# Kernel optimization log

Measured on AMD Instinct MI355X. Metric: run time of the kernel, lower is better.

The kernel has to match this reference:

```python
import jax, jax.numpy as jnp
import numpy as np

B, N, T, D, S = 2, 16384, 2048, 128, 384
NW, WQ, H, L, NH = 512, 32, 128, 3, 4
NTOK = 33  # len(const.tokens)


def _ln(x):
    m = x.mean(-1, keepdims=True)
    v = x.var(-1, keepdims=True)
    return (x - m) * jax.lax.rsqrt(v + 1e-5)


def setup_inputs() -> dict:
    key = jax.random.key(0)
    ks = jax.random.split(key, 24)
    sc = 0.02
    a = jax.random.normal(ks[0], (B, T, S), jnp.float32)
    q = jax.random.normal(ks[1], (B, N, D), jnp.float32)
    c = jax.random.normal(ks[2], (B, N, D), jnp.float32)
    atom_dec_bias = jax.random.normal(ks[3], (B, NW, NH, WQ, H), jnp.float32) * 0.1
    # one-hot atom->token map: ~8 atoms per token
    tok_idx = jnp.arange(N) // (N // T)
    atom_to_token = jnp.tile(jax.nn.one_hot(tok_idx, T, dtype=jnp.float32)[None], (B, 1, 1))
    atom_mask = jnp.ones((B, N), jnp.float32)
    # windowed key indices: 128-atom neighborhood centered on each 32-atom window
    starts = np.clip(np.arange(NW) * WQ + WQ // 2 - H // 2, 0, N - H)
    key_idx = jnp.asarray(starts[:, None] + np.arange(H)[None, :], jnp.int32)
    nrm = lambda k, shp: jax.random.normal(k, shp, jnp.float32) * sc
    p = {
        'a_to_q_w': nrm(ks[4], (S, D)),
        'Wq': nrm(ks[5], (L, D, D)), 'Wk': nrm(ks[6], (L, D, D)), 'Wv': nrm(ks[7], (L, D, D)),
        'Wg': nrm(ks[8], (L, D, D)), 'Wo': nrm(ks[9], (L, D, D)),
        'Wcs': nrm(ks[10], (L, D, D)), 'Wcb': nrm(ks[11], (L, D, D)), 'Wog': nrm(ks[12], (L, D, D)),
        'Wcs2': nrm(ks[13], (L, D, D)), 'Wcb2': nrm(ks[14], (L, D, D)), 'Wog2': nrm(ks[15], (L, D, D)),
        'W1': nrm(ks[16], (L, D, 2 * D)), 'W2': nrm(ks[17], (L, D, 2 * D)), 'W3': nrm(ks[18], (L, 2 * D, D)),
        'ln_g': jnp.ones((D,), jnp.float32), 'ln_b': jnp.zeros((D,), jnp.float32),
        'Wpos': nrm(ks[19], (D, 3)), 'Wres': nrm(ks[20], (D, NTOK)), 'bres': jnp.zeros((NTOK,), jnp.float32),
    }
    return dict(a=a, q=q, c=c, atom_dec_bias=atom_dec_bias, atom_to_token=atom_to_token,
                atom_mask=atom_mask, key_idx=key_idx, **p)


def reference(a, q, c, atom_dec_bias, atom_to_token, atom_mask, key_idx,
              a_to_q_w, Wq, Wk, Wv, Wg, Wo, Wcs, Wcb, Wog, Wcs2, Wcb2, Wog2,
              W1, W2, W3, ln_g, ln_b, Wpos, Wres, bres):
    Bq, Nq, Dq = q.shape
    nw, h = key_idx.shape
    wq = Nq // nw
    nh = atom_dec_bias.shape[2]
    dh = Dq // nh
    # token -> atom broadcast (dense bmm over one-hot == gather)
    q = q + jnp.einsum('bnt,btd->bnd', atom_to_token, a @ a_to_q_w)
    cn = _ln(c)
    mbias = (1.0 - atom_mask[:, key_idx])[:, :, None, None, :] * -1e9  # (B,NW,1,1,H)
    depth = Wq.shape[0]
    for l in range(depth):
        # AdaLN conditioning on c
        hcur = _ln(q) * jax.nn.sigmoid(cn @ Wcs[l]) + cn @ Wcb[l]
        qh = (hcur @ Wq[l]).reshape(Bq, nw, wq, nh, dh)
        hk = hcur[:, key_idx]  # (B,NW,H,D) gather = to_keys
        kh = (hk @ Wk[l]).reshape(Bq, nw, h, nh, dh)
        vh = (hk @ Wv[l]).reshape(Bq, nw, h, nh, dh)
        scores = jnp.einsum('bwqhd,bwkhd->bwhqk', qh, kh) / (dh ** 0.5) + atom_dec_bias + mbias
        attn = jax.nn.softmax(scores, axis=-1)
        o = jnp.einsum('bwhqk,bwkhd->bwqhd', attn, vh).reshape(Bq, Nq, Dq)
        o = jax.nn.sigmoid(hcur @ Wg[l]) * o
        q = q + jax.nn.sigmoid(cn @ Wog[l]) * (o @ Wo[l])
        # conditioned transition (SwiGLU)
        h2 = _ln(q) * jax.nn.sigmoid(cn @ Wcs2[l]) + cn @ Wcb2[l]
        ff = (jax.nn.silu(h2 @ W1[l]) * (h2 @ W2[l])) @ W3[l]
        q = q + jax.nn.sigmoid(cn @ Wog2[l]) * ff
    # atom -> residue scatter_add pooling
    tok_idx = jnp.argmax(atom_to_token, axis=-1)  # (B,N) int
    src = q * atom_mask[..., None]
    nt = atom_to_token.shape[-1]
    s_feat = jax.vmap(lambda s, i: jax.ops.segment_sum(s, i, num_segments=nt))(src, tok_idx)
    res_type = s_feat @ Wres + bres
    # LayerNorm + Linear position head
    r_update = (_ln(q) * ln_g + ln_b) @ Wpos
    return (r_update, res_type)
```

## Files before the change

kernel.cpp:

```cpp
#include <hip/hip_runtime.h>

typedef unsigned short u16;
typedef u16 u16x4 __attribute__((ext_vector_type(4)));
typedef u16 u16x8 __attribute__((ext_vector_type(8)));
typedef __bf16 bf16x8 __attribute__((ext_vector_type(8)));
typedef float f32x4 __attribute__((ext_vector_type(4)));

#define B_  2
#define N_  16384
#define T_  2048
#define D_  128
#define S_  384
#define NW_ 512
#define WQ_ 32
#define H_  128
#define L_  3
#define NH_ 4
#define NTOK_ 33
#define BN_ (B_*N_)

__device__ __forceinline__ float b2f(u16 u) {
    return __builtin_bit_cast(float, ((unsigned)u) << 16);
}
__device__ __forceinline__ u16 f2b(float f) {
    unsigned x = __builtin_bit_cast(unsigned, f);
    unsigned r = x + 0x7fffu + ((x >> 16) & 1u);
    return (u16)(r >> 16);
}
__device__ __forceinline__ float sigf(float x) { return 1.f / (1.f + __expf(-x)); }
__device__ __forceinline__ float ldin(const void* p, size_t i, int f) {
    return f ? ((const float*)p)[i] : b2f(((const u16*)p)[i]);
}

enum { M_STORE = 0, M_CBSG = 1, M_F32 = 2, M_RESID = 3, M_RESLN = 4 };

__global__ void sentinel_k(float* out, float v) { if (threadIdx.x == 0) out[0] = v; }

__global__ __launch_bounds__(64) void detect_k(const u16* __restrict__ a, int* flag)
{
    int t = threadIdx.x;
    u16 u = a[2 * t];
    int e = (u >> 7) & 0xFF;
    bool inval = (u != 0) && (e < 96 || e > 143);
    unsigned long long m = __ballot(inval);
    if (t == 0) flag[0] = (__popcll(m) >= 6) ? 1 : 0;
}

template<bool FUSE_LN>
__global__ __launch_bounds__(256) void gemm_k(
    const u16* __restrict__ A, int lda, int asrc,
    const u16* __restrict__ WT, int K,
    u16* __restrict__ C, int ldc,
    const u16* __restrict__ E1, int e1ld,
    float* __restrict__ QF,
    const u16* __restrict__ SG, const u16* __restrict__ CB, int sgcbld,
    u16* __restrict__ HC, int mode, const int* __restrict__ dtf)
{
    __shared__ __align__(16) char smem[FUSE_LN ? 65536 : 36864];
    u16 (*As)[72] = (u16(*)[72])smem;
    u16 (*Bs)[72] = (u16(*)[72])(smem + 18432);
    float (*Tf)[128] = (float(*)[128])smem;

    const int tid = threadIdx.x;
    const int m0 = blockIdx.x * 128, n0 = blockIdx.y * 128;
    const int lane = tid & 63, wid = tid >> 6;
    const int wr = (wid >> 1) * 64, wc = (wid & 1) * 64;
    const int lr = lane & 15, lq = lane >> 4;
    const int af32 = (asrc == 1 && dtf) ? dtf[0] : 0;

    f32x4 zero4 = {0.f, 0.f, 0.f, 0.f};
    f32x4 acc[4][4];
#pragma unroll
    for (int i = 0; i < 4; ++i)
#pragma unroll
        for (int j = 0; j < 4; ++j) acc[i][j] = zero4;

    for (int kt = 0; kt < K; kt += 64) {
#pragma unroll
        for (int i = 0; i < 4; ++i) {
            int id = tid + i * 256;
            int r = id >> 3, c = (id & 7) * 8;
            if (asrc == 2) {
                size_t ab = (size_t)(m0 + r) * 512 + kt + c;
                u16x8 u1 = *(const u16x8*)&A[ab];
                u16x8 u2 = *(const u16x8*)&A[ab + 256];
                u16x8 t;
#pragma unroll
                for (int j = 0; j < 8; ++j) {
                    float x = b2f(u1[j]);
                    t[j] = f2b(x * sigf(x) * b2f(u2[j]));
                }
                *(u16x8*)&As[r][c] = t;
            } else if (af32) {
                const float* Af = (const float*)A;
                size_t ai = (size_t)(m0 + r) * lda + kt + c;
                f32x4 p0 = *(const f32x4*)&Af[ai];
                f32x4 p1 = *(const f32x4*)&Af[ai + 4];
                u16x8 t;
                t[0] = f2b(p0[0]); t[1] = f2b(p0[1]); t[2] = f2b(p0[2]); t[3] = f2b(p0[3]);
                t[4] = f2b(p1[0]); t[5] = f2b(p1[1]); t[6] = f2b(p1[2]); t[7] = f2b(p1[3]);
                *(u16x8*)&As[r][c] = t;
            } else {
                *(u16x8*)&As[r][c] = *(const u16x8*)&A[(size_t)(m0 + r) * lda + kt + c];
            }
            *(u16x8*)&Bs[r][c] = *(const u16x8*)&WT[(size_t)(n0 + r) * K + kt + c];
        }
        __syncthreads();
#pragma unroll
        for (int ks = 0; ks < 2; ++ks) {
            bf16x8 af[4], bfr[4];
#pragma unroll
            for (int t = 0; t < 4; ++t) {
                af[t]  = *(const bf16x8*)&As[wr + t * 16 + lr][ks * 32 + lq * 8];
                bfr[t] = *(const bf16x8*)&Bs[wc + t * 16 + lr][ks * 32 + lq * 8];
            }
#pragma unroll
            for (int mt = 0; mt < 4; ++mt)
#pragma unroll
                for (int nt = 0; nt < 4; ++nt)
                    acc[mt][nt] = __builtin_amdgcn_mfma_f32_16x16x32_bf16(
                        bfr[nt], af[mt], acc[mt][nt], 0, 0, 0);
        }
        __syncthreads();
    }

    const bool sig_half = (n0 >= 768);
#pragma unroll
    for (int mt = 0; mt < 4; ++mt)
#pragma unroll
        for (int nt = 0; nt < 4; ++nt) {
            int lm = wr + mt * 16 + lr;
            int lnb = wc + nt * 16 + lq * 4;
            int m = m0 + lm;
            size_t o = (size_t)m * ldc + n0 + lnb;
            f32x4 v = acc[mt][nt];
            if (mode == M_STORE) {
                u16x4 t = {f2b(v[0]), f2b(v[1]), f2b(v[2]), f2b(v[3])};
                *(u16x4*)&C[o] = t;
            } else if (mode == M_CBSG) {
                u16x4 t;
#pragma unroll
                for (int r = 0; r < 4; ++r) t[r] = f2b(sig_half ? sigf(v[r]) : v[r]);
                *(u16x4*)&C[o] = t;
            } else if (mode == M_F32) {
                *(f32x4*)&QF[o] = v;
            } else {
                f32x4 q = *(const f32x4*)&QF[o];
                u16x4 e = *(const u16x4*)&E1[(size_t)m * e1ld + n0 + lnb];
#pragma unroll
                for (int r = 0; r < 4; ++r) q[r] += b2f(e[r]) * v[r];
                *(f32x4*)&QF[o] = q;
                if (FUSE_LN) *(f32x4*)&Tf[lm][lnb] = q;
            }
        }

    if (FUSE_LN && mode == M_RESLN) {
        __syncthreads();
        int g = tid >> 4, li = tid & 15;
#pragma unroll
        for (int rr = 0; rr < 8; ++rr) {
            int lm = g * 8 + rr;
            float x[8];
            float s = 0.f, sq = 0.f;
#pragma unroll
            for (int j = 0; j < 8; ++j) {
                x[j] = Tf[lm][li * 8 + j];
                s += x[j]; sq += x[j] * x[j];
            }
#pragma unroll
            for (int off = 1; off < 16; off <<= 1) {
                s  += __shfl_xor(s, off, 64);
                sq += __shfl_xor(sq, off, 64);
            }
            float mu = s * (1.f / 128.f);
            float var = sq * (1.f / 128.f) - mu * mu;
            float inv = rsqrtf(fmaxf(var, 0.f) + 1e-5f);
            int grow = m0 + lm;
            size_t sb = (size_t)grow * sgcbld;
            u16x8 hv;
#pragma unroll
            for (int j = 0; j < 8; ++j) {
                int col = li * 8 + j;
                hv[j] = f2b((x[j] - mu) * inv * b2f(SG[sb + col]) + b2f(CB[sb + col]));
            }
            *(u16x8*)&HC[(size_t)grow * 128 + li * 8] = hv;
        }
    }
}

__global__ __launch_bounds__(256) void attn_k(
    const u16* __restrict__ proj,
    const u16* __restrict__ biasbf,
    const void* __restrict__ mask,
    const int* __restrict__ key_idx,
    u16* __restrict__ o_out,
    const int* __restrict__ dtf)
{
    __shared__ __align__(16) u16 Ks[128][128];
    __shared__ __align__(16) u16 Vt[128][128];
    const int tid = threadIdx.x;
    const int b = blockIdx.x >> 9, w = blockIdx.x & 511;
    int raw = key_idx[w * 128];
    if ((unsigned)raw > (unsigned)(N_ - H_))
        raw = (int)__builtin_bit_cast(float, raw);
    const int ks0 = raw < 0 ? 0 : (raw > N_ - H_ ? N_ - H_ : raw);
    const int lane = tid & 63, h = tid >> 6;
    const int lr = lane & 15, lq = lane >> 4;
    const int hoff = h * 32;
    const int f = dtf[0];

#pragma unroll
    for (int i = 0; i < 8; ++i) {
        int id = tid + i * 256;
        int r = id >> 4, c = (id & 15) * 8;
        size_t gbase = ((size_t)(b * N_ + ks0 + r)) * 512;
        *(u16x8*)&Ks[r][c] = *(const u16x8*)&proj[gbase + 128 + c];
        u16x8 v = *(const u16x8*)&proj[gbase + 256 + c];
#pragma unroll
        for (int j = 0; j < 8; ++j) Vt[c + j][r] = v[j];
    }
    __syncthreads();

    bf16x8 aq[2];
#pragma unroll
    for (int mt = 0; mt < 2; ++mt) {
        int qa = w * 32 + mt * 16 + lr;
        aq[mt] = *(const bf16x8*)&proj[((size_t)(b * N_ + qa)) * 512 + hoff + lq * 8];
    }
    f32x4 zero4 = {0.f, 0.f, 0.f, 0.f};
    f32x4 s[2][8];
#pragma unroll
    for (int nt = 0; nt < 8; ++nt) {
        bf16x8 bk = *(const bf16x8*)&Ks[nt * 16 + lr][hoff + lq * 8];
        s[0][nt] = __builtin_amdgcn_mfma_f32_16x16x32_bf16(aq[0], bk, zero4, 0, 0, 0);
        s[1][nt] = __builtin_amdgcn_mfma_f32_16x16x32_bf16(aq[1], bk, zero4, 0, 0, 0);
    }

    const float scl = 0.17677669529663687f;
    float mb[8];
#pragma unroll
    for (int nt = 0; nt < 8; ++nt)
        mb[nt] = (1.f - ldin(mask, (size_t)b * N_ + ks0 + nt * 16 + lr, f)) * -1e9f;
    size_t bb = (((size_t)b * 512 + w) * 4 + h) * (size_t)(32 * 128);
#pragma unroll
    for (int mt = 0; mt < 2; ++mt)
#pragma unroll
        for (int nt = 0; nt < 8; ++nt)
#pragma unroll
            for (int r = 0; r < 4; ++r) {
                int qq = mt * 16 + lq * 4 + r;
                int kk = nt * 16 + lr;
                s[mt][nt][r] = s[mt][nt][r] * scl + b2f(biasbf[bb + qq * 128 + kk]) + mb[nt];
            }

#pragma unroll
    for (int mt = 0; mt < 2; ++mt)
#pragma unroll
        for (int r = 0; r < 4; ++r) {
            float mx = -3.4e38f;
#pragma unroll
            for (int nt = 0; nt < 8; ++nt) mx = fmaxf(mx, s[mt][nt][r]);
#pragma unroll
            for (int off = 1; off < 16; off <<= 1) mx = fmaxf(mx, __shfl_xor(mx, off, 64));
            float sm = 0.f;
#pragma unroll
            for (int nt = 0; nt < 8; ++nt) {
                float p = __expf(s[mt][nt][r] - mx);
                s[mt][nt][r] = p; sm += p;
            }
#pragma unroll
            for (int off = 1; off < 16; off <<= 1) sm += __shfl_xor(sm, off, 64);
            float inv = 1.f / sm;
#pragma unroll
            for (int nt = 0; nt < 8; ++nt) s[mt][nt][r] *= inv;
        }

    __syncthreads();
#pragma unroll
    for (int mt = 0; mt < 2; ++mt)
#pragma unroll
        for (int nt = 0; nt < 8; ++nt)
#pragma unroll
            for (int r = 0; r < 4; ++r)
                Ks[hoff + mt * 16 + lq * 4 + r][nt * 16 + lr] = f2b(s[mt][nt][r]);
    __syncthreads();

    f32x4 o[2][2];
    o[0][0] = zero4; o[0][1] = zero4; o[1][0] = zero4; o[1][1] = zero4;
#pragma unroll
    for (int kst = 0; kst < 4; ++kst) {
        bf16x8 ap[2], bv[2];
#pragma unroll
        for (int mt = 0; mt < 2; ++mt)
            ap[mt] = *(const bf16x8*)&Ks[hoff + mt * 16 + lr][kst * 32 + lq * 8];
#pragma unroll
        for (int nt = 0; nt < 2; ++nt)
            bv[nt] = *(const bf16x8*)&Vt[hoff + nt * 16 + lr][kst * 32 + lq * 8];
#pragma unroll
        for (int mt = 0; mt < 2; ++mt)
#pragma unroll
            for (int nt = 0; nt < 2; ++nt)
                o[mt][nt] = __builtin_amdgcn_mfma_f32_16x16x32_bf16(ap[mt], bv[nt], o[mt][nt], 0, 0, 0);
    }

#pragma unroll
    for (int mt = 0; mt < 2; ++mt)
#pragma unroll
        for (int nt = 0; nt < 2; ++nt)
#pragma unroll
            for (int r = 0; r < 4; ++r) {
                int qa = w * 32 + mt * 16 + lq * 4 + r;
                int d = hoff + nt * 16 + lr;
                size_t gi = ((size_t)(b * N_ + qa)) * 512 + 384 + d;
                float g = sigf(b2f(proj[gi]));
                o_out[((size_t)(b * N_ + qa)) * 128 + d] = f2b(g * o[mt][nt][r]);
            }
}

struct TJob { const void* base; int off; int dst; int K; int N; };
struct TJobs { TJob j[43]; };
__global__ __launch_bounds__(256) void prologue_k(
    const void* __restrict__ bias_in, u16* __restrict__ biasbf,
    const void* __restrict__ c_in, u16* __restrict__ cn,
    TJobs jobs, u16* __restrict__ wt, const int* __restrict__ dtf)
{
    __shared__ __align__(16) u16 Ls[64][72];
    int bx = blockIdx.x;
    int f = dtf[0];
    if (bx < 8192) {
        size_t i = ((size_t)bx * 256 + threadIdx.x) * 8;
        if (f) {
            const float* s = (const float*)bias_in;
            f32x4 p0 = *(const f32x4*)&s[i];
            f32x4 p1 = *(const f32x4*)&s[i + 4];
            u16x8 t;
            t[0] = f2b(p0[0]); t[1] = f2b(p0[1]); t[2] = f2b(p0[2]); t[3] = f2b(p0[3]);
            t[4] = f2b(p1[0]); t[5] = f2b(p1[1]); t[6] = f2b(p1[2]); t[7] = f2b(p1[3]);
            *(u16x8*)&biasbf[i] = t;
        } else {
            *(u16x8*)&biasbf[i] = *(const u16x8*)&((const u16*)bias_in)[i];
        }
    } else if (bx < 16384) {
        int row = (bx - 8192) * 4 + (threadIdx.x >> 6);
        int l = threadIdx.x & 63;
        size_t base = (size_t)row * 128;
        float a = ldin(c_in, base + l, f), b = ldin(c_in, base + l + 64, f);
        float s = a + b, ss = a * a + b * b;
#pragma unroll
        for (int off = 1; off < 64; off <<= 1) {
            s  += __shfl_xor(s, off, 64);
            ss += __shfl_xor(ss, off, 64);
        }
        float m = s * (1.f / 128.f);
        float v = ss * (1.f / 128.f) - m * m;
        float inv = rsqrtf(fmaxf(v, 0.f) + 1e-5f);
        cn[base + l]      = f2b((a - m) * inv);
        cn[base + l + 64] = f2b((b - m) * inv);
    } else {
        int t = bx - 16384;
        int jidx = t / 12, tidx = t - jidx * 12;
        TJob jb = jobs.j[jidx];
        int ntk = jb.K >> 6, ntn = jb.N >> 6;
        if (tidx >= ntk * ntn) return;
        int kt = (tidx % ntk) << 6;
        int nt = (tidx / ntk) << 6;
        int r = threadIdx.x >> 3, cc = (threadIdx.x & 7) * 8;
#pragma unroll
        for (int p = 0; p < 2; ++p) {
            int kl = r + p * 32;
            size_t si = (size_t)jb.off + (size_t)(kt + kl) * jb.N + nt + cc;
            u16x8 v;
            if (f) {
                const float* s = (const float*)jb.base;
                f32x4 p0 = *(const f32x4*)&s[si];
                f32x4 p1 = *(const f32x4*)&s[si + 4];
                v[0] = f2b(p0[0]); v[1] = f2b(p0[1]); v[2] = f2b(p0[2]); v[3] = f2b(p0[3]);
                v[4] = f2b(p1[0]); v[5] = f2b(p1[1]); v[6] = f2b(p1[2]); v[7] = f2b(p1[3]);
            } else {
                v = *(const u16x8*)&((const u16*)jb.base)[si];
            }
            *(u16x8*)&Ls[kl][cc] = v;
        }
        __syncthreads();
#pragma unroll
        for (int p = 0; p < 2; ++p) {
            int nl = r + p * 32;
            u16x8 w;
#pragma unroll
            for (int j = 0; j < 8; ++j) w[j] = Ls[cc + j][nl];
            *(u16x8*)&wt[(size_t)jb.dst + (size_t)(nt + nl) * jb.K + kt + cc] = w;
        }
    }
}

__global__ __launch_bounds__(256) void initq_ln_k(
    const void* __restrict__ qin, const float* __restrict__ aw,
    float* __restrict__ qf,
    const u16* __restrict__ cs0, const u16* __restrict__ cb0, int sgcbld,
    u16* __restrict__ hcur, const int* __restrict__ dtf)
{
    int an = blockIdx.x * 4 + (threadIdx.x >> 6);
    int l = threadIdx.x & 63;
    int f = dtf[0];
    int b = an >> 14, n = an & 16383, t = n >> 3;
    size_t base = (size_t)an * 128;
    size_t ab = ((size_t)b * T_ + t) * 128;
    float a0 = ldin(qin, base + l, f)      + aw[ab + l];
    float a1 = ldin(qin, base + l + 64, f) + aw[ab + l + 64];
    qf[base + l] = a0; qf[base + l + 64] = a1;
    float s = a0 + a1, ss = a0 * a0 + a1 * a1;
#pragma unroll
    for (int off = 1; off < 64; off <<= 1) {
        s  += __shfl_xor(s, off, 64);
        ss += __shfl_xor(ss, off, 64);
    }
    float m = s * (1.f / 128.f);
    float v = ss * (1.f / 128.f) - m * m;
    float inv = rsqrtf(fmaxf(v, 0.f) + 1e-5f);
    size_t sb = (size_t)an * sgcbld;
    hcur[base + l]      = f2b((a0 - m) * inv * b2f(cs0[sb + l])      + b2f(cb0[sb + l]));
    hcur[base + l + 64] = f2b((a1 - m) * inv * b2f(cs0[sb + l + 64]) + b2f(cb0[sb + l + 64]));
}

__global__ __launch_bounds__(256) void final_k(const float* __restrict__ q,
    const void* __restrict__ ln_g, const void* __restrict__ ln_b,
    const void* __restrict__ Wpos,
    const void* __restrict__ mask, const void* __restrict__ Wres,
    const void* __restrict__ bres,
    float* __restrict__ out1, float* __restrict__ out2,
    const int* __restrict__ dtf)
{
    int f = dtf[0];
    int bx = blockIdx.x;
    if (bx < 8192) {
        int row = bx * 4 + (threadIdx.x >> 6);
        int l = threadIdx.x & 63;
        size_t base = (size_t)row * 128;
        float a = q[base + l], b = q[base + l + 64];
        float s = a + b, ss = a * a + b * b;
#pragma unroll
        for (int off = 1; off < 64; off <<= 1) {
            s  += __shfl_xor(s, off, 64);
            ss += __shfl_xor(ss, off, 64);
        }
        float m = s * (1.f / 128.f);
        float v = ss * (1.f / 128.f) - m * m;
        float inv = rsqrtf(fmaxf(v, 0.f) + 1e-5f);
        float y0 = (a - m) * inv * ldin(ln_g, l, f)      + ldin(ln_b, l, f);
        float y1 = (b - m) * inv * ldin(ln_g, l + 64, f) + ldin(ln_b, l + 64, f);
        float p0 = y0 * ldin(Wpos, l * 3 + 0, f) + y1 * ldin(Wpos, (l + 64) * 3 + 0, f);
        float p1 = y0 * ldin(Wpos, l * 3 + 1, f) + y1 * ldin(Wpos, (l + 64) * 3 + 1, f);
        float p2 = y0 * ldin(Wpos, l * 3 + 2, f) + y1 * ldin(Wpos, (l + 64) * 3 + 2, f);
#pragma unroll
        for (int off = 1; off < 64; off <<= 1) {
            p0 += __shfl_xor(p0, off, 64);
            p1 += __shfl_xor(p1, off, 64);
            p2 += __shfl_xor(p2, off, 64);
        }
        if (l == 0) {
            out1[(size_t)row * 3 + 0] = p0;
            out1[(size_t)row * 3 + 1] = p1;
            out1[(size_t)row * 3 + 2] = p2;
        }
    } else {
        __shared__ float sfeat[4][128];
        int wid = threadIdx.x >> 6, l = threadIdx.x & 63;
        int tok = (bx - 8192) * 4 + wid;
        int b = tok >> 11, t = tok & 2047;
        float a0 = 0.f, a1 = 0.f;
#pragma unroll
        for (int i = 0; i < 8; ++i) {
            size_t an = (size_t)b * N_ + t * 8 + i;
            float mk = ldin(mask, an, f);
            a0 += q[an * 128 + l] * mk;
            a1 += q[an * 128 + l + 64] * mk;
        }
        sfeat[wid][l] = a0; sfeat[wid][l + 64] = a1;
        __builtin_amdgcn_s_waitcnt(0);
        if (l < NTOK_) {
            float r = ldin(bres, l, f);
            for (int d = 0; d < 128; ++d) r += sfeat[wid][d] * ldin(Wres, d * NTOK_ + l, f);
            out2[(size_t)tok * NTOK_ + l] = r;
        }
    }
}

extern "C" void kernel_launch(void* const* d_in, const int* in_sizes, int n_in,
                              void* d_out, int out_size, void* d_ws, size_t ws_size,
                              hipStream_t stream)
{
    (void)out_size;
    float* out = (float*)d_out;
    const size_t WS_NEED = 295698432;

    static const int EXP_SZ[27] = {
        1572864, 4194304, 4194304, 16777216, 67108864, 32768, 65536,
        49152, 49152, 49152, 49152, 49152, 49152,
        49152, 49152, 49152, 49152, 49152, 49152,
        98304, 98304, 98304, 128, 128, 384, 4224, 33 };
    int bad = -1;
    int ncheck = n_in < 27 ? n_in : 27;
    for (int i = 0; i < ncheck; ++i)
        if (in_sizes[i] != EXP_SZ[i]) { bad = i; break; }
    if (bad >= 0) { sentinel_k<<<1, 64, 0, stream>>>(out, 256.0f * (bad + 1)); return; }
    if (n_in < 27) { sentinel_k<<<1, 64, 0, stream>>>(out, 8192.0f); return; }
    if (ws_size < WS_NEED) { sentinel_k<<<1, 64, 0, stream>>>(out, 12288.0f); return; }

    const void* a_in    = d_in[0];
    const void* q_in    = d_in[1];
    const void* c_in    = d_in[2];
    const void* bias_in = d_in[3];
    const void* mask_in = d_in[5];
    const int*  kidx    = (const int*)d_in[6];
    const void* a2q  = d_in[7];
    const void* Wq   = d_in[8];
    const void* Wk   = d_in[9];
    const void* Wv   = d_in[10];
    const void* Wg   = d_in[11];
    const void* Wo   = d_in[12];
    const void* Wcs  = d_in[13];
    const void* Wcb  = d_in[14];
    const void* Wog  = d_in[15];
    const void* Wcs2 = d_in[16];
    const void* Wcb2 = d_in[17];
    const void* Wog2 = d_in[18];
    const void* W1   = d_in[19];
    const void* W2   = d_in[20];
    const void* W3   = d_in[21];
    const void* ln_g = d_in[22];
    const void* ln_b = d_in[23];
    const void* Wpos = d_in[24];
    const void* Wres = d_in[25];
    const void* bres = d_in[26];

    char* ws = (char*)d_ws;
    u16*   wt     = (u16*)ws;
    int*   flag   = (int*)(ws + 2088960);
    float* qf     = (float*)(ws + 2097152);
    u16*   cn     = (u16*)(ws + 18874368);
    u16*   biasbf = (u16*)(ws + 27262976);
    u16*   cnproj = (u16*)(ws + 60817408);
    u16*   hcur   = (u16*)(ws + 211812352);
    u16*   proj   = (u16*)(ws + 220200960);
    u16*   obuf   = (u16*)(ws + 253755392);
    u16*   u12    = (u16*)(ws + 262144000);
    float* aw     = (float*)(ws + 262144000);

    detect_k<<<1, 64, 0, stream>>>((const u16*)a_in, flag);

    TJobs jobs; int nj = 0;
    for (int l = 0; l < 3; ++l) {
        jobs.j[nj++] = {Wq,   l * 16384, l * 65536 + 0,     128, 128};
        jobs.j[nj++] = {Wk,   l * 16384, l * 65536 + 16384, 128, 128};
        jobs.j[nj++] = {Wv,   l * 16384, l * 65536 + 32768, 128, 128};
        jobs.j[nj++] = {Wg,   l * 16384, l * 65536 + 49152, 128, 128};
        jobs.j[nj++] = {Wcb,  l * 16384, 196608 + l * 16384,       128, 128};
        jobs.j[nj++] = {Wcb2, l * 16384, 196608 + (3 + l) * 16384, 128, 128};
        jobs.j[nj++] = {Wcs,  l * 16384, 294912 + l * 16384,       128, 128};
        jobs.j[nj++] = {Wog,  l * 16384, 294912 + (3 + l) * 16384, 128, 128};
        jobs.j[nj++] = {Wcs2, l * 16384, 294912 + (6 + l) * 16384, 128, 128};
        jobs.j[nj++] = {Wog2, l * 16384, 294912 + (9 + l) * 16384, 128, 128};
        jobs.j[nj++] = {W1,   l * 32768, 491520 + l * 65536,         128, 256};
        jobs.j[nj++] = {W2,   l * 32768, 491520 + l * 65536 + 32768, 128, 256};
        jobs.j[nj++] = {W3,   l * 32768, 688128 + l * 32768, 256, 128};
        jobs.j[nj++] = {Wo,   l * 16384, 835584 + l * 16384, 128, 128};
    }
    jobs.j[nj++] = {a2q, 0, 786432, 384, 128};

    prologue_k<<<16384 + 43 * 12, 256, 0, stream>>>(bias_in, biasbf, c_in, cn, jobs, wt, flag);
    gemm_k<false><<<dim3(32, 1), 256, 0, stream>>>(
        (const u16*)a_in, S_, 1, wt + 786432, S_, nullptr, D_,
        nullptr, 0, aw, nullptr, nullptr, 0, nullptr, M_F32, flag);
    gemm_k<false><<<dim3(256, 18), 256, 0, stream>>>(
        cn, D_, 0, wt + 196608, D_, cnproj, 2304,
        nullptr, 0, nullptr, nullptr, nullptr, 0, nullptr, M_CBSG, nullptr);
    initq_ln_k<<<8192, 256, 0, stream>>>(q_in, aw, qf,
        cnproj + 768, cnproj + 0, 2304, hcur, flag);

    for (int l = 0; l < 3; ++l) {
        const u16* wt_proj = wt + l * 65536;
        const u16* wt_w12  = wt + 491520 + l * 65536;
        const u16* wt_w3   = wt + 688128 + l * 32768;
        const u16* wt_wo   = wt + 835584 + l * 16384;
        const u16* cb2_l = cnproj + 384 + l * 128;
        const u16* og_l  = cnproj + 1152 + l * 128;
        const u16* cs2_l = cnproj + 1536 + l * 128;
        const u16* og2_l = cnproj + 1920 + l * 128;
        const u16* cs_n  = cnproj + 768 + (l + 1) * 128;
        const u16* cb_n  = cnproj + 0 + (l + 1) * 128;

        gemm_k<false><<<dim3(256, 4), 256, 0, stream>>>(
            hcur, D_, 0, wt_proj, D_, proj, 512,
            nullptr, 0, nullptr, nullptr, nullptr, 0, nullptr, M_STORE, nullptr);
        attn_k<<<1024, 256, 0, stream>>>(proj, biasbf, mask_in, kidx, obuf, flag);
        gemm_k<true><<<dim3(256, 1), 256, 0, stream>>>(
            obuf, D_, 0, wt_wo, D_, nullptr, D_,
            og_l, 2304, qf, cs2_l, cb2_l, 2304, hcur, M_RESLN, nullptr);
        gemm_k<false><<<dim3(256, 4), 256, 0, stream>>>(
            hcur, D_, 0, wt_w12, D_, u12, 512,
            nullptr, 0, nullptr, nullptr, nullptr, 0, nullptr, M_STORE, nullptr);
        if (l < 2)
            gemm_k<true><<<dim3(256, 1), 256, 0, stream>>>(
                u12, 512, 2, wt_w3, 256, nullptr, D_,
                og2_l, 2304, qf, cs_n, cb_n, 2304, hcur, M_RESLN, nullptr);
        else
            gemm_k<false><<<dim3(256, 1), 256, 0, stream>>>(
                u12, 512, 2, wt_w3, 256, nullptr, D_,
                og2_l, 2304, qf, nullptr, nullptr, 0, nullptr, M_RESID, nullptr);
    }

    final_k<<<9216, 256, 0, stream>>>(qf, ln_g, ln_b, Wpos, mask_in, Wres, bres,
                                      out, out + (size_t)BN_ * 3, flag);
}
```

Measured before the change: 981.2 us.

## Fuse follow-on projection GEMMs into residual+LayerNorm GEMM epilogue

The residual+LN GEMM epilogue now keeps the normalized 128-row tile in shared memory and immediately multiplies it by the next weight matrix (W1|W2 or the next layer's QKVG projection), writing u12/proj directly. This removes the separate projection GEMM launches and the hcur write/read round-trip. The trade-off is lower parallelism: each 128-row block now serially computes 512 output columns with only 256 blocks, instead of spreading that work over 1024 blocks.

Measured after the change: 941.4 us. 1.04x faster.

```diff
diff --git a/kernel.cpp b/kernel.cpp
--- a/kernel.cpp
+++ b/kernel.cpp
@@ -54,7 +54,8 @@
     const u16* __restrict__ E1, int e1ld,
     float* __restrict__ QF,
     const u16* __restrict__ SG, const u16* __restrict__ CB, int sgcbld,
-    u16* __restrict__ HC, int mode, const int* __restrict__ dtf)
+    u16* __restrict__ HC, int mode, const int* __restrict__ dtf,
+    const u16* __restrict__ WT2, u16* __restrict__ C2, int ldc2, int n2)
 {
     __shared__ __align__(16) char smem[FUSE_LN ? 65536 : 36864];
     u16 (*As)[72] = (u16(*)[72])smem;
@@ -157,6 +158,7 @@
     if (FUSE_LN && mode == M_RESLN) {
         __syncthreads();
         int g = tid >> 4, li = tid & 15;
+        u16x8 hvr[8];
 #pragma unroll
         for (int rr = 0; rr < 8; ++rr) {
             int lm = g * 8 + rr;
@@ -183,7 +185,62 @@
                 int col = li * 8 + j;
                 hv[j] = f2b((x[j] - mu) * inv * b2f(SG[sb + col]) + b2f(CB[sb + col]));
             }
-            *(u16x8*)&HC[(size_t)grow * 128 + li * 8] = hv;
+            hvr[rr] = hv;
+            if (HC) *(u16x8*)&HC[(size_t)grow * 128 + li * 8] = hv;
+        }
+
+        if (n2 > 0) {
+            __syncthreads();
+            u16 (*Hs)[136] = (u16(*)[136])smem;
+            u16 (*Bs2)[72] = (u16(*)[72])(smem + 36864);
+#pragma unroll
+            for (int rr = 0; rr < 8; ++rr)
+                *(u16x8*)&Hs[g * 8 + rr][li * 8] = hvr[rr];
+
+            for (int nc = 0; nc < n2; nc += 128) {
+                f32x4 acc2[4][4];
+#pragma unroll
+                for (int i = 0; i < 4; ++i)
+#pragma unroll
+                    for (int j = 0; j < 4; ++j) acc2[i][j] = zero4;
+#pragma unroll
+                for (int kt2 = 0; kt2 < 128; kt2 += 64) {
+                    __syncthreads();
+#pragma unroll
+                    for (int i = 0; i < 4; ++i) {
+                        int id = tid + i * 256;
+                        int r = id >> 3, c = (id & 7) * 8;
+                        *(u16x8*)&Bs2[r][c] =
+                            *(const u16x8*)&WT2[(size_t)(nc + r) * 128 + kt2 + c];
+                    }
+                    __syncthreads();
+#pragma unroll
+                    for (int ks = 0; ks < 2; ++ks) {
+                        bf16x8 af[4], bfr[4];
+#pragma unroll
+                        for (int t = 0; t < 4; ++t) {
+                            af[t]  = *(const bf16x8*)&Hs[wr + t * 16 + lr][kt2 + ks * 32 + lq * 8];
+                            bfr[t] = *(const bf16x8*)&Bs2[wc + t * 16 + lr][ks * 32 + lq * 8];
+                        }
+#pragma unroll
+                        for (int mt = 0; mt < 4; ++mt)
+#pragma unroll
+                            for (int nt = 0; nt < 4; ++nt)
+                                acc2[mt][nt] = __builtin_amdgcn_mfma_f32_16x16x32_bf16(
+                                    bfr[nt], af[mt], acc2[mt][nt], 0, 0, 0);
+                    }
+                }
+#pragma unroll
+                for (int mt = 0; mt < 4; ++mt)
+#pragma unroll
+                    for (int nt = 0; nt < 4; ++nt) {
+                        int m = m0 + wr + mt * 16 + lr;
+                        int n = nc + wc + nt * 16 + lq * 4;
+                        f32x4 v = acc2[mt][nt];
+                        u16x4 t = {f2b(v[0]), f2b(v[1]), f2b(v[2]), f2b(v[3])};
+                        *(u16x4*)&C2[(size_t)m * ldc2 + n] = t;
+                    }
+            }
         }
     }
 }
@@ -570,15 +627,22 @@
     prologue_k<<<16384 + 43 * 12, 256, 0, stream>>>(bias_in, biasbf, c_in, cn, jobs, wt, flag);
     gemm_k<false><<<dim3(32, 1), 256, 0, stream>>>(
         (const u16*)a_in, S_, 1, wt + 786432, S_, nullptr, D_,
-        nullptr, 0, aw, nullptr, nullptr, 0, nullptr, M_F32, flag);
+        nullptr, 0, aw, nullptr, nullptr, 0, nullptr, M_F32, flag,
+        nullptr, nullptr, 0, 0);
     gemm_k<false><<<dim3(256, 18), 256, 0, stream>>>(
         cn, D_, 0, wt + 196608, D_, cnproj, 2304,
-        nullptr, 0, nullptr, nullptr, nullptr, 0, nullptr, M_CBSG, nullptr);
+        nullptr, 0, nullptr, nullptr, nullptr, 0, nullptr, M_CBSG, nullptr,
+        nullptr, nullptr, 0, 0);
     initq_ln_k<<<8192, 256, 0, stream>>>(q_in, aw, qf,
         cnproj + 768, cnproj + 0, 2304, hcur, flag);
 
+    gemm_k<false><<<dim3(256, 4), 256, 0, stream>>>(
+        hcur, D_, 0, wt + 0 * 65536, D_, proj, 512,
+        nullptr, 0, nullptr, nullptr, nullptr, 0, nullptr, M_STORE, nullptr,
+        nullptr, nullptr, 0, 0);
+
     for (int l = 0; l < 3; ++l) {
-        const u16* wt_proj = wt + l * 65536;
+        const u16* wt_proj_n = wt + (l + 1) * 65536;
         const u16* wt_w12  = wt + 491520 + l * 65536;
         const u16* wt_w3   = wt + 688128 + l * 32768;
         const u16* wt_wo   = wt + 835584 + l * 16384;
@@ -589,24 +653,21 @@
         const u16* cs_n  = cnproj + 768 + (l + 1) * 128;
         const u16* cb_n  = cnproj + 0 + (l + 1) * 128;
 
-        gemm_k<false><<<dim3(256, 4), 256, 0, stream>>>(
-            hcur, D_, 0, wt_proj, D_, proj, 512,
-            nullptr, 0, nullptr, nullptr, nullptr, 0, nullptr, M_STORE, nullptr);
         attn_k<<<1024, 256, 0, stream>>>(proj, biasbf, mask_in, kidx, obuf, flag);
         gemm_k<true><<<dim3(256, 1), 256, 0, stream>>>(
             obuf, D_, 0, wt_wo, D_, nullptr, D_,
-            og_l, 2304, qf, cs2_l, cb2_l, 2304, hcur, M_RESLN, nullptr);
-        gemm_k<false><<<dim3(256, 4), 256, 0, stream>>>(
-            hcur, D_, 0, wt_w12, D_, u12, 512,
-            nullptr, 0, nullptr, nullptr, nullptr, 0, nullptr, M_STORE, nullptr);
+            og_l, 2304, qf, cs2_l, cb2_l, 2304, nullptr, M_RESLN, nullptr,
+            wt_w12, u12, 512, 512);
         if (l < 2)
             gemm_k<true><<<dim3(256, 1), 256, 0, stream>>>(
                 u12, 512, 2, wt_w3, 256, nullptr, D_,
-                og2_l, 2304, qf, cs_n, cb_n, 2304, hcur, M_RESLN, nullptr);
+                og2_l, 2304, qf, cs_n, cb_n, 2304, nullptr, M_RESLN, nullptr,
+                wt_proj_n, proj, 512, 512);
         else
             gemm_k<false><<<dim3(256, 1), 256, 0, stream>>>(
                 u12, 512, 2, wt_w3, 256, nullptr, D_,
-                og2_l, 2304, qf, nullptr, nullptr, 0, nullptr, M_RESID, nullptr);
+                og2_l, 2304, qf, nullptr, nullptr, 0, nullptr, M_RESID, nullptr,
+                nullptr, nullptr, 0, 0);
     }
 
     final_k<<<9216, 256, 0, stream>>>(qf, ln_g, ln_b, Wpos, mask_in, Wres, bres,
```
